# Kernel optimization log

Measured on AMD Instinct MI355X. Metric: run time of the kernel, lower is better.

Reference implementation:

```python
import jax, jax.numpy as jnp
import numpy as np

D_MODEL = 2048
NUM_HEADS = 16
D_Q = 1536
D_KV = 512
BS, SL = 2, 2048


def _lin(x, w, b):
    # torch nn.Linear: y = x @ w.T + b, w: [out, in]
    return jnp.einsum('...i,oi->...o', x, w) + b


def _freqs(seq_len, dim, theta=10000.0):
    # Faithful to source incl. precedence quirk: tn = 1 / ((theta ** arange) / dim).
    # float32 overflow -> inf -> tn = 0 for large exponents (identity rotation).
    exps = jnp.arange(0, dim, 2, dtype=jnp.float32)
    tn = 1.0 / ((theta ** exps) / dim)
    m = jnp.arange(seq_len, dtype=jnp.float32)
    ang = jnp.outer(m, tn)  # [sl, dim/2]
    return jnp.cos(ang), jnp.sin(ang)


def _rope(x, cos, sin):
    # x: [bs, sl, dim]; complex pairs are (x[..., 2i], x[..., 2i+1])
    xe = x[..., 0::2]
    xo = x[..., 1::2]
    re = xe * cos - xo * sin
    im = xe * sin + xo * cos
    return jnp.stack([re, im], axis=-1).reshape(x.shape)


def _init_linear(key, out_f, in_f):
    k1, k2 = jax.random.split(key)
    bound = 1.0 / np.sqrt(in_f)
    w = jax.random.uniform(k1, (out_f, in_f), jnp.float32, -bound, bound)
    b = jax.random.uniform(k2, (out_f,), jnp.float32, -bound, bound)
    return w, b


def setup_inputs() -> dict:
    key = jax.random.key(0)
    ks = jax.random.split(key, 9)
    x = jax.random.normal(ks[0], (BS, SL, D_MODEL), jnp.float32)
    w_down_q, b_down_q = _init_linear(ks[1], D_Q, D_MODEL)
    w_up_q, b_up_q = _init_linear(ks[2], D_MODEL, D_Q)
    w_down_kv, b_down_kv = _init_linear(ks[3], D_KV, D_MODEL)
    w_up_k, b_up_k = _init_linear(ks[4], D_MODEL, D_KV)
    w_up_v, b_up_v = _init_linear(ks[5], D_MODEL, D_KV)
    wq_r, bq_r = _init_linear(ks[6], D_MODEL, D_Q)
    wk_r, bk_r = _init_linear(ks[7], D_MODEL, D_KV)
    wo, bo = _init_linear(ks[8], D_MODEL, D_MODEL)
    return dict(x=x,
                w_down_q=w_down_q, b_down_q=b_down_q,
                w_up_q=w_up_q, b_up_q=b_up_q,
                w_down_kv=w_down_kv, b_down_kv=b_down_kv,
                w_up_k=w_up_k, b_up_k=b_up_k,
                w_up_v=w_up_v, b_up_v=b_up_v,
                wq_r=wq_r, bq_r=bq_r,
                wk_r=wk_r, bk_r=bk_r,
                wo=wo, bo=bo)


def reference(x, w_down_q, b_down_q, w_up_q, b_up_q, w_down_kv, b_down_kv,
              w_up_k, b_up_k, w_up_v, b_up_v, wq_r, bq_r, wk_r, bk_r, wo, bo):
    bs, sl, dim = x.shape
    nh, hd = NUM_HEADS, dim // NUM_HEADS
    cos, sin = _freqs(sl, dim)

    # Query path: down-proj -> up-proj content + decoupled RoPE branch
    ct_q = _lin(x, w_down_q, b_down_q)                       # [bs, sl, d_q]
    q_ct = _lin(ct_q, w_up_q, b_up_q)                        # [bs, sl, d_model]
    rope_q = _rope(_lin(ct_q, wq_r, bq_r), cos, sin)         # [bs, sl, d_model]
    q = (q_ct + rope_q).reshape(bs, sl, nh, hd)

    # KV path: shared latent -> separate K/V up-proj + RoPE branch on K
    ct_kv = _lin(x, w_down_kv, b_down_kv)                    # [bs, sl, d_kv]
    k_ct = _lin(ct_kv, w_up_k, b_up_k)
    rope_k = _rope(_lin(ct_kv, wk_r, bk_r), cos, sin)
    k = (k_ct + rope_k).reshape(bs, sl, nh, hd)
    v = _lin(ct_kv, w_up_v, b_up_v).reshape(bs, sl, nh, hd)

    # Attention: explicit matmul + softmax + matmul (no causal mask in source)
    scores = jnp.einsum('bqhd,bkhd->bhqk', q, k) / np.sqrt(hd)
    probs = jax.nn.softmax(scores, axis=-1)
    a = jnp.einsum('bhqk,bkhd->bqhd', probs, v).reshape(bs, sl, nh * hd)
    return _lin(a, wo, bo)
```

## Files before the change

kernel.cpp:

```cpp
#include <hip/hip_runtime.h>

typedef float f32x4 __attribute__((ext_vector_type(4)));
typedef float f32x16 __attribute__((ext_vector_type(16)));
typedef unsigned short us8 __attribute__((ext_vector_type(8)));

#define DEVINL __device__ __forceinline__

DEVINL unsigned short f2bf(float f) {
  unsigned u = __builtin_bit_cast(unsigned, f);
  u += 0x7fffu + ((u >> 16) & 1u);
  return (unsigned short)(u >> 16);
}
DEVINL float bf2f(unsigned short b) { return __builtin_bit_cast(float, ((unsigned)b) << 16); }
DEVINL us8 ld8(const unsigned short* p) { return *reinterpret_cast<const us8*>(p); }
DEVINL void mfma16(f32x4& acc, us8 a, us8 b) {
  asm("v_mfma_f32_16x16x32_bf16 %0, %1, %2, %0" : "+v"(acc) : "v"(a), "v"(b));
}
DEVINL void mfma32(f32x16& acc, us8 a, us8 b) {
  asm("v_mfma_f32_32x32x16_bf16 %0, %1, %2, %0" : "+v"(acc) : "v"(a), "v"(b));
}
DEVINL unsigned cvtpk_bf16(float lo, float hi) {
  unsigned r;
  asm("v_cvt_pk_bf16_f32 %0, %1, %2" : "=v"(r) : "v"(lo), "v"(hi));
  return r;
}
DEVINL us8 us8_from4(unsigned a, unsigned b, unsigned c, unsigned d) {
  union { unsigned u[4]; us8 v; } x;
  x.u[0] = a; x.u[1] = b; x.u[2] = c; x.u[3] = d;
  return x.v;
}
DEVINL void gld16(const void* g, void* l) {
  __builtin_amdgcn_global_load_lds((const __attribute__((address_space(1))) void*)g,
                                   (__attribute__((address_space(3))) void*)l, 16, 0, 0);
}

DEVINL void cvt4(const float* __restrict__ s, unsigned short* __restrict__ d, long i) {
  float4 v = reinterpret_cast<const float4*>(s)[i];
  unsigned lo = (unsigned)f2bf(v.x) | ((unsigned)f2bf(v.y) << 16);
  unsigned hi = (unsigned)f2bf(v.z) | ((unsigned)f2bf(v.w) << 16);
  reinterpret_cast<uint2*>(d)[i] = make_uint2(lo, hi);
}

__global__ void k_prep(const float* __restrict__ x, const float* __restrict__ wdq,
                       const float* __restrict__ wdkv, const float* __restrict__ wuq,
                       const float* __restrict__ wqr, const float* __restrict__ wuk,
                       const float* __restrict__ wkr, const float* __restrict__ wuv,
                       const float* __restrict__ wo, const float* __restrict__ bdq,
                       const float* __restrict__ bdkv, const float* __restrict__ buq,
                       const float* __restrict__ bqr, const float* __restrict__ buk,
                       const float* __restrict__ bkr, const float* __restrict__ buv,
                       unsigned short* __restrict__ xb, unsigned short* __restrict__ wcd,
                       unsigned short* __restrict__ wcq, unsigned short* __restrict__ wck,
                       unsigned short* __restrict__ wob, float* __restrict__ cosT,
                       float* __restrict__ sinT, float* __restrict__ bcd,
                       float* __restrict__ bcq, float* __restrict__ bck) {
  constexpr long C0 = 2097152, C1 = C0 + 786432, C2 = C1 + 262144, C3 = C2 + 786432,
                 C4 = C3 + 786432, C5 = C4 + 262144, C6 = C5 + 262144, C7 = C6 + 262144,
                 C8 = C7 + 1048576, C9 = C8 + 2097152, C10 = C9 + 3072;
  long u = (long)blockIdx.x * 256 + threadIdx.x;
  if (u < C0) cvt4(x, xb, u);
  else if (u < C1) cvt4(wdq, wcd, u - C0);
  else if (u < C2) cvt4(wdkv, wcd + 1536L * 2048, u - C1);
  else if (u < C3) cvt4(wuq, wcq, u - C2);
  else if (u < C4) cvt4(wqr, wcq + 2048L * 1536, u - C3);
  else if (u < C5) cvt4(wuk, wck, u - C4);
  else if (u < C6) cvt4(wkr, wck + 2048L * 512, u - C5);
  else if (u < C7) cvt4(wuv, wck + 4096L * 512, u - C6);
  else if (u < C8) cvt4(wo, wob, u - C7);
  else if (u < C9) {
    long idx = u - C8;
    int s = (int)(idx >> 10), i = (int)(idx & 1023);
    float e = (float)(2 * i);
    float pw = powf(10000.0f, e);
    float tn = 1.0f / (pw / 2048.0f);
    float ang = (float)s * tn;
    cosT[idx] = cosf(ang);
    sinT[idx] = sinf(ang);
  } else if (u < C10) {
    long j4 = (u - C9) * 4;
#pragma unroll
    for (int k = 0; k < 4; ++k) {
      long j = j4 + k;
      if (j < 2048) {
        bcd[j] = j < 1536 ? bdq[j] : bdkv[j - 1536];
      } else if (j < 6144) {
        long jj = j - 2048;
        bcq[jj] = jj < 2048 ? buq[jj] : bqr[jj - 2048];
      } else {
        long jj = j - 6144;
        bck[jj] = jj < 2048 ? buk[jj] : (jj < 4096 ? bkr[jj - 2048] : buv[jj - 4096]);
      }
    }
  }
}

template <int BN, bool OUTF32>
__global__ __launch_bounds__(BN) void k_gemm256(const unsigned short* __restrict__ A,
                                                const unsigned short* __restrict__ B,
                                                const float* __restrict__ bias,
                                                void* __restrict__ Cout, int N, int K, int lda) {
  constexpr int THREADS = BN;
  constexpr int WN = BN / 128;
  constexpr int NA = 512 / THREADS;
  constexpr int NB = BN * 4 / THREADS;
  constexpr int SLOT = 128 * 32 + BN * 32;
  __shared__ unsigned short lds[3 * SLOT];
  const int nwg = gridDim.x;
  const int orig = blockIdx.x;
  const int wgid = (orig & 7) * (nwg >> 3) + (orig >> 3);
  const int nbn = N / BN;
  const int bn = wgid % nbn, bm = wgid / nbn;
  const int tid = threadIdx.x, lane = tid & 63, w = tid >> 6;
  const int g = lane >> 4, l16 = lane & 15;
  const int wm = w / WN, wn = w % WN;
  f32x4 acc[4][8] = {};
  const unsigned short* Abase = A + (size_t)bm * 128 * lda;
  const unsigned short* Bbase = B + (size_t)bn * BN * K;
  size_t aoff[NA], boff[NB];
#pragma unroll
  for (int j = 0; j < NA; ++j) {
    int c = j * THREADS + tid;
    int row = c >> 2, gc = (c & 3) ^ ((row >> 1) & 3);
    aoff[j] = (size_t)row * lda + gc * 8;
  }
#pragma unroll
  for (int j = 0; j < NB; ++j) {
    int cb = j * THREADS + tid;
    int row = cb >> 2, gc = (cb & 3) ^ ((row >> 1) & 3);
    boff[j] = (size_t)row * K + gc * 8;
  }
  auto STAGE = [&](int slot, int kt) {
    unsigned short* s = &lds[slot * SLOT];
#pragma unroll
    for (int j = 0; j < NA; ++j) gld16(Abase + aoff[j] + kt, s + (j * THREADS + tid) * 8);
#pragma unroll
    for (int j = 0; j < NB; ++j)
      gld16(Bbase + boff[j] + kt, s + 128 * 32 + (j * THREADS + tid) * 8);
  };
  const int nt = K >> 5;
  STAGE(0, 0);
  STAGE(1, 32);
  if (BN == 256) asm volatile("s_waitcnt vmcnt(6)" ::: "memory");
  else           asm volatile("s_waitcnt vmcnt(8)" ::: "memory");
  asm volatile("s_barrier" ::: "memory");
  for (int t = 0; t < nt; ++t) {
    const int slot = t % 3;
    if (t + 2 < nt) STAGE((t + 2) % 3, (t + 2) * 32);
    const unsigned short* sa = &lds[slot * SLOT];
    const unsigned short* sb = sa + 128 * 32;
    us8 af[4], bf[8];
#pragma unroll
    for (int m = 0; m < 4; ++m) {
      int row = wm * 64 + m * 16 + l16;
      af[m] = ld8(&sa[row * 32 + ((g ^ ((row >> 1) & 3)) * 8)]);
    }
#pragma unroll
    for (int n = 0; n < 8; ++n) {
      int row = wn * 128 + n * 16 + l16;
      bf[n] = ld8(&sb[row * 32 + ((g ^ ((row >> 1) & 3)) * 8)]);
    }
    __builtin_amdgcn_s_setprio(1);
#pragma unroll
    for (int m = 0; m < 4; ++m)
#pragma unroll
      for (int n = 0; n < 8; ++n) mfma16(acc[m][n], af[m], bf[n]);
    __builtin_amdgcn_s_setprio(0);
    if (t < nt - 2) {
      if (BN == 256) asm volatile("s_waitcnt vmcnt(6)" ::: "memory");
      else           asm volatile("s_waitcnt vmcnt(8)" ::: "memory");
    } else {
      asm volatile("s_waitcnt vmcnt(0)" ::: "memory");
    }
    asm volatile("s_barrier" ::: "memory");
  }
#pragma unroll
  for (int n = 0; n < 8; ++n) {
    int col = bn * BN + wn * 128 + n * 16 + l16;
    float bv = bias[col];
#pragma unroll
    for (int m = 0; m < 4; ++m) {
      int row0 = bm * 128 + wm * 64 + m * 16 + g * 4;
#pragma unroll
      for (int r = 0; r < 4; ++r) {
        float vv = acc[m][n][r] + bv;
        if (OUTF32)
          reinterpret_cast<float*>(Cout)[(size_t)(row0 + r) * N + col] = vv;
        else
          reinterpret_cast<unsigned short*>(Cout)[(size_t)(row0 + r) * N + col] = f2bf(vv);
      }
    }
  }
}

__global__ void k_rope_combine(const unsigned short* __restrict__ src, int ldin,
                               const float* __restrict__ cosT, const float* __restrict__ sinT,
                               unsigned short* __restrict__ outp) {
  int pidx = blockIdx.x * 256 + threadIdx.x;
  if (pidx >= 4096 * 1024) return;
  int row = pidx >> 10, i = pidx & 1023;
  int s = row & 2047;
  float c = cosT[s * 1024 + i], sn = sinT[s * 1024 + i];
  const unsigned short* rp = src + (size_t)row * ldin;
  float xe = bf2f(rp[2048 + 2 * i]), xo = bf2f(rp[2048 + 2 * i + 1]);
  float re = xe * c - xo * sn;
  float im = xe * sn + xo * c;
  float q0 = bf2f(rp[2 * i]) + re;
  float q1 = bf2f(rp[2 * i + 1]) + im;
  unsigned pack = (unsigned)f2bf(q0) | ((unsigned)f2bf(q1) << 16);
  *reinterpret_cast<unsigned*>(&outp[(size_t)row * 2048 + 2 * i]) = pack;
}

__global__ __launch_bounds__(256) void k_transpose_v(const unsigned short* __restrict__ v, int ld,
                                                     unsigned short* __restrict__ vt) {
  __shared__ unsigned short t[32][33];
  int tx = threadIdx.x & 31, ty = threadIdx.x >> 5;
  int r0 = blockIdx.y * 32, c0 = blockIdx.x * 32;
#pragma unroll
  for (int jj = 0; jj < 4; ++jj)
    t[ty * 4 + jj][tx] = v[(size_t)(r0 + ty * 4 + jj) * ld + c0 + tx];
  __syncthreads();
  int b = r0 >> 11;
#pragma unroll
  for (int jj = 0; jj < 4; ++jj) {
    int colc = c0 + ty * 4 + jj;
    size_t orow = (size_t)(b * 16 + (colc >> 7)) * 128 + (colc & 127);
    vt[orow * 2048 + (r0 & 2047) + tx] = t[tx][ty * 4 + jj];
  }
}

__global__ __launch_bounds__(256, 2) void k_attn(const unsigned short* __restrict__ Qsrc,
                                                 const unsigned short* __restrict__ Kg,
                                                 const unsigned short* __restrict__ VT,
                                                 const float* __restrict__ cosT,
                                                 const float* __restrict__ sinT,
                                                 unsigned short* __restrict__ Aout) {
  __shared__ unsigned short Ks[2][64 * 128];
  __shared__ unsigned short VTs[2][128 * 64];
  const int tid = threadIdx.x, lane = tid & 63, w = tid >> 6;
  const int hh = lane >> 5, q32 = lane & 31;
  const int orig = blockIdx.x;
  const int wgid = (orig & 7) * 64 + (orig >> 3);
  const int qt = wgid & 15;
  const int hb = wgid >> 4;
  const int h = hb & 15, b = hb >> 4;
  const float SC2 = 0.08838834764831845f * 1.4426950408889634f;
  const int srow = qt * 128 + w * 32 + q32;
  us8 qf[8];
  {
    const unsigned short* Qr = Qsrc + ((size_t)b * 2048 + srow) * 4096;
#pragma unroll
    for (int ds = 0; ds < 8; ++ds) {
      int dcol = h * 128 + ds * 16 + hh * 8;
      us8 c8 = ld8(&Qr[dcol]);
      us8 r8 = ld8(&Qr[2048 + dcol]);
      unsigned wv[4];
#pragma unroll
      for (int p2 = 0; p2 < 4; ++p2) {
        int i = (dcol >> 1) + p2;
        float cc = cosT[srow * 1024 + i], ss = sinT[srow * 1024 + i];
        float xe = bf2f(r8[2 * p2]), xo = bf2f(r8[2 * p2 + 1]);
        float o0 = (bf2f(c8[2 * p2]) + xe * cc - xo * ss) * SC2;
        float o1 = (bf2f(c8[2 * p2 + 1]) + xe * ss + xo * cc) * SC2;
        wv[p2] = cvtpk_bf16(o0, o1);
      }
      qf[ds] = us8_from4(wv[0], wv[1], wv[2], wv[3]);
    }
  }
  f32x16 O[4] = {};
  float mq = -1e30f, lq = 0.f;
  const unsigned short* Kbase = Kg + (size_t)b * 2048 * 2048 + h * 128;
  const unsigned short* VTb = VT + (size_t)(b * 16 + h) * 128 * 2048;
  auto STAGE = [&](int bufi, int ktrow) {
#pragma unroll
    for (int j = 0; j < 4; ++j) {
      int ch = (j * 4 + w) * 64 + lane;
      int key = ch >> 4, cp = ch & 15;
      gld16(&Kbase[(size_t)(ktrow + key) * 2048 + (size_t)((cp ^ (key & 15)) * 8)],
            &Ks[bufi][(j * 4 + w) * 512]);
      int d = ch >> 3, c2 = ch & 7;
      gld16(&VTb[(size_t)d * 2048 + ktrow + (size_t)((c2 ^ (d & 7)) * 8)],
            &VTs[bufi][(j * 4 + w) * 512]);
    }
  };
  STAGE(0, 0);
  for (int t = 0; t < 32; ++t) {
    const int cur = t & 1;
    __syncthreads();
    if (t < 31) STAGE(cur ^ 1, (t + 1) * 64);
    f32x16 S2[2] = {};
    __builtin_amdgcn_s_setprio(1);
#pragma unroll
    for (int kb = 0; kb < 2; ++kb) {
      const int key = kb * 32 + q32;
      const int swz = key & 15;
#pragma unroll
      for (int ds = 0; ds < 8; ++ds) {
        us8 kf = ld8(&Ks[cur][key * 128 + (((ds * 2 + hh) ^ swz) * 8)]);
        mfma32(S2[kb], kf, qf[ds]);
      }
    }
    __builtin_amdgcn_s_setprio(0);
    float mx[16];
#pragma unroll
    for (int r = 0; r < 16; ++r) mx[r] = fmaxf(S2[0][r], S2[1][r]);
#pragma unroll
    for (int st = 8; st > 0; st >>= 1)
#pragma unroll
      for (int r = 0; r < st; ++r) mx[r] = fmaxf(mx[r], mx[r + st]);
    float smax = fmaxf(mx[0], __shfl_xor(mx[0], 32));
    if (!__all(smax <= mq + 8.0f)) {
      float mn = fmaxf(mq, smax);
      float fac = exp2f(mq - mn);
      lq *= fac;
      mq = mn;
#pragma unroll
      for (int r = 0; r < 16; ++r) {
        int qr = (r & 3) + 8 * (r >> 2) + 4 * hh;
        float fr = __shfl(fac, qr);
#pragma unroll
        for (int db = 0; db < 4; ++db) O[db][r] *= fr;
      }
    }
    float ps = 0.f;
    unsigned pk[2][8];
#pragma unroll
    for (int kb = 0; kb < 2; ++kb) {
      float e[16];
#pragma unroll
      for (int r = 0; r < 16; ++r) {
        e[r] = exp2f(S2[kb][r] - mq);
        ps += e[r];
      }
#pragma unroll
      for (int pp = 0; pp < 8; ++pp) pk[kb][pp] = cvtpk_bf16(e[2 * pp], e[2 * pp + 1]);
    }
    ps += __shfl_xor(ps, 32);
    lq += ps;
    __builtin_amdgcn_s_setprio(1);
#pragma unroll
    for (int ks = 0; ks < 4; ++ks) {
      const int kb = ks >> 1, kk = ks & 1;
      unsigned u_own = hh ? pk[kb][4 * kk + 2] : pk[kb][4 * kk + 0];
      unsigned v_own = hh ? pk[kb][4 * kk + 3] : pk[kb][4 * kk + 1];
      unsigned u_snd = hh ? pk[kb][4 * kk + 0] : pk[kb][4 * kk + 2];
      unsigned v_snd = hh ? pk[kb][4 * kk + 1] : pk[kb][4 * kk + 3];
      unsigned uo = (unsigned)__shfl_xor((int)u_snd, 32);
      unsigned vo = (unsigned)__shfl_xor((int)v_snd, 32);
      us8 pa = us8_from4(hh ? uo : u_own, hh ? vo : v_own, hh ? u_own : uo, hh ? v_own : vo);
#pragma unroll
      for (int db = 0; db < 4; ++db) {
        int d = db * 32 + q32;
        us8 vf = ld8(&VTs[cur][d * 64 + (((ks * 2 + hh) ^ (d & 7)) * 8)]);
        mfma32(O[db], pa, vf);
      }
    }
    __builtin_amdgcn_s_setprio(0);
  }
  float inv = 1.0f / lq;
#pragma unroll
  for (int r = 0; r < 16; ++r) {
    int qr = (r & 3) + 8 * (r >> 2) + 4 * hh;
    float ir = __shfl(inv, qr);
    size_t row = (size_t)b * 2048 + qt * 128 + w * 32 + qr;
#pragma unroll
    for (int db = 0; db < 4; ++db)
      Aout[row * 2048 + h * 128 + db * 32 + q32] = f2bf(O[db][r] * ir);
  }
}

extern "C" void kernel_launch(void* const* d_in, const int* in_sizes, int n_in, void* d_out,
                              int out_size, void* d_ws, size_t ws_size, hipStream_t stream) {
  (void)in_sizes; (void)n_in; (void)out_size; (void)ws_size;
  constexpr int Mr = 4096;
  using US = unsigned short;
  const float* x        = (const float*)d_in[0];
  const float* w_down_q = (const float*)d_in[1];
  const float* b_down_q = (const float*)d_in[2];
  const float* w_up_q   = (const float*)d_in[3];
  const float* b_up_q   = (const float*)d_in[4];
  const float* w_down_kv= (const float*)d_in[5];
  const float* b_down_kv= (const float*)d_in[6];
  const float* w_up_k   = (const float*)d_in[7];
  const float* b_up_k   = (const float*)d_in[8];
  const float* w_up_v   = (const float*)d_in[9];
  const float* b_up_v   = (const float*)d_in[10];
  const float* wq_r     = (const float*)d_in[11];
  const float* bq_r     = (const float*)d_in[12];
  const float* wk_r     = (const float*)d_in[13];
  const float* bk_r     = (const float*)d_in[14];
  const float* wo       = (const float*)d_in[15];
  const float* bo       = (const float*)d_in[16];

  char* p = (char*)d_ws;
  auto alloc = [&](size_t bytes) { char* r = p; p += (bytes + 255) & ~(size_t)255; return r; };
  float* cosT      = (float*)alloc((size_t)2048 * 1024 * 4);
  float* sinT      = (float*)alloc((size_t)2048 * 1024 * 4);
  US* wcat_kvup    = (US*)alloc((size_t)6144 * 512 * 2);
  US* wob          = (US*)alloc((size_t)2048 * 2048 * 2);
  US* ct           = (US*)alloc((size_t)Mr * 2048 * 2);
  US* t12          = (US*)alloc((size_t)Mr * 4096 * 2);
  US* vtb          = (US*)alloc((size_t)Mr * 2048 * 2);
  US* kb           = (US*)alloc((size_t)Mr * 2048 * 2);
  float* bcat_down = (float*)alloc(2048 * 4);
  float* bcat_qup  = (float*)alloc(4096 * 4);
  float* bcat_kvup = (float*)alloc(6144 * 4);
  US* xb           = (US*)alloc((size_t)Mr * 2048 * 2);
  US* wcat_down    = (US*)alloc((size_t)2048 * 2048 * 2);
  US* wcat_qup     = (US*)alloc((size_t)4096 * 1536 * 2);
  alloc((size_t)12 * 1024 * 1024);
  US* kv3  = xb;
  US* aout = ct;

  k_prep<<<dim3(33804), dim3(256), 0, stream>>>(
      x, w_down_q, w_down_kv, w_up_q, wq_r, w_up_k, wk_r, w_up_v, wo, b_down_q, b_down_kv,
      b_up_q, bq_r, b_up_k, bk_r, b_up_v, xb, wcat_down, wcat_qup, wcat_kvup, wob, cosT, sinT,
      bcat_down, bcat_qup, bcat_kvup);

  k_gemm256<128, false><<<dim3((2048 / 128) * (Mr / 128)), dim3(128), 0, stream>>>(
      xb, wcat_down, bcat_down, (void*)ct, 2048, 2048, 2048);
  k_gemm256<256, false><<<dim3((4096 / 256) * (Mr / 128)), dim3(256), 0, stream>>>(
      ct, wcat_qup, bcat_qup, (void*)t12, 4096, 1536, 2048);
  k_gemm256<256, false><<<dim3((6144 / 256) * (Mr / 128)), dim3(256), 0, stream>>>(
      ct + 1536, wcat_kvup, bcat_kvup, (void*)kv3, 6144, 512, 2048);
  k_rope_combine<<<dim3((4096 * 1024 + 255) / 256), dim3(256), 0, stream>>>(kv3, 6144, cosT, sinT,
                                                                            kb);
  k_transpose_v<<<dim3(64, 128), dim3(256), 0, stream>>>(kv3 + 4096, 6144, vtb);
  k_attn<<<dim3(512), dim3(256), 0, stream>>>(t12, kb, vtb, cosT, sinT, aout);
  k_gemm256<128, true><<<dim3((2048 / 128) * (Mr / 128)), dim3(128), 0, stream>>>(
      aout, wob, bo, d_out, 2048, 2048, 2048);
}
```

Measured before the change: 359.1 us.

## Split attention KV range across two workgroups and merge partial softmax results

The attention kernel is split along the key dimension into two halves, doubling the grid to 1024 workgroups. Each half writes unnormalized fp32 partial outputs plus running max and sum, and a new merge kernel combines them into bf16. LDS double buffering is replaced with a single buffer and an extra barrier, allowing up to 4 workgroups per CU. This adds fp32 partial-output traffic (written into d_out and kv3 scratch) and an extra launch, and staging loads are no longer overlapped with compute.

```diff
diff --git a/kernel.cpp b/kernel.cpp
--- a/kernel.cpp
+++ b/kernel.cpp
@@ -228,20 +228,24 @@
   }
 }
 
-__global__ __launch_bounds__(256, 2) void k_attn(const unsigned short* __restrict__ Qsrc,
+__global__ __launch_bounds__(256, 4) void k_attn(const unsigned short* __restrict__ Qsrc,
                                                  const unsigned short* __restrict__ Kg,
                                                  const unsigned short* __restrict__ VT,
                                                  const float* __restrict__ cosT,
                                                  const float* __restrict__ sinT,
-                                                 unsigned short* __restrict__ Aout) {
-  __shared__ unsigned short Ks[2][64 * 128];
-  __shared__ unsigned short VTs[2][128 * 64];
+                                                 float* __restrict__ Op0,
+                                                 float* __restrict__ Op1,
+                                                 float2* __restrict__ ml0,
+                                                 float2* __restrict__ ml1) {
+  __shared__ unsigned short Ks[64 * 128];
+  __shared__ unsigned short VTs[128 * 64];
   const int tid = threadIdx.x, lane = tid & 63, w = tid >> 6;
   const int hh = lane >> 5, q32 = lane & 31;
   const int orig = blockIdx.x;
-  const int wgid = (orig & 7) * 64 + (orig >> 3);
-  const int qt = wgid & 15;
-  const int hb = wgid >> 4;
+  const int wgid = (orig & 7) * 128 + (orig >> 3);
+  const int half = wgid & 1;
+  const int qt = (wgid >> 1) & 15;
+  const int hb = wgid >> 5;
   const int h = hb & 15, b = hb >> 4;
   const float SC2 = 0.08838834764831845f * 1.4426950408889634f;
   const int srow = qt * 128 + w * 32 + q32;
@@ -270,23 +274,23 @@
   float mq = -1e30f, lq = 0.f;
   const unsigned short* Kbase = Kg + (size_t)b * 2048 * 2048 + h * 128;
   const unsigned short* VTb = VT + (size_t)(b * 16 + h) * 128 * 2048;
-  auto STAGE = [&](int bufi, int ktrow) {
+  auto STAGE = [&](int ktrow) {
 #pragma unroll
     for (int j = 0; j < 4; ++j) {
       int ch = (j * 4 + w) * 64 + lane;
       int key = ch >> 4, cp = ch & 15;
       gld16(&Kbase[(size_t)(ktrow + key) * 2048 + (size_t)((cp ^ (key & 15)) * 8)],
-            &Ks[bufi][(j * 4 + w) * 512]);
+            &Ks[(j * 4 + w) * 512]);
       int d = ch >> 3, c2 = ch & 7;
       gld16(&VTb[(size_t)d * 2048 + ktrow + (size_t)((c2 ^ (d & 7)) * 8)],
-            &VTs[bufi][(j * 4 + w) * 512]);
+            &VTs[(j * 4 + w) * 512]);
     }
   };
-  STAGE(0, 0);
-  for (int t = 0; t < 32; ++t) {
-    const int cur = t & 1;
+  const int t0 = half * 16;
+  for (int tt = 0; tt < 16; ++tt) {
     __syncthreads();
-    if (t < 31) STAGE(cur ^ 1, (t + 1) * 64);
+    STAGE((t0 + tt) * 64);
+    __syncthreads();
     f32x16 S2[2] = {};
     __builtin_amdgcn_s_setprio(1);
 #pragma unroll
@@ -295,7 +299,7 @@
       const int swz = key & 15;
 #pragma unroll
       for (int ds = 0; ds < 8; ++ds) {
-        us8 kf = ld8(&Ks[cur][key * 128 + (((ds * 2 + hh) ^ swz) * 8)]);
+        us8 kf = ld8(&Ks[key * 128 + (((ds * 2 + hh) ^ swz) * 8)]);
         mfma32(S2[kb], kf, qf[ds]);
       }
     }
@@ -350,22 +354,46 @@
 #pragma unroll
       for (int db = 0; db < 4; ++db) {
         int d = db * 32 + q32;
-        us8 vf = ld8(&VTs[cur][d * 64 + (((ks * 2 + hh) ^ (d & 7)) * 8)]);
+        us8 vf = ld8(&VTs[d * 64 + (((ks * 2 + hh) ^ (d & 7)) * 8)]);
         mfma32(O[db], pa, vf);
       }
     }
     __builtin_amdgcn_s_setprio(0);
   }
-  float inv = 1.0f / lq;
+  float* Op = half ? Op1 : Op0;
+  const size_t rbase = (size_t)b * 2048 + qt * 128 + w * 32;
 #pragma unroll
   for (int r = 0; r < 16; ++r) {
     int qr = (r & 3) + 8 * (r >> 2) + 4 * hh;
-    float ir = __shfl(inv, qr);
-    size_t row = (size_t)b * 2048 + qt * 128 + w * 32 + qr;
 #pragma unroll
     for (int db = 0; db < 4; ++db)
-      Aout[row * 2048 + h * 128 + db * 32 + q32] = f2bf(O[db][r] * ir);
-  }
+      Op[(rbase + qr) * 2048 + h * 128 + db * 32 + q32] = O[db][r];
+  }
+  if (hh == 0) {
+    float2* ml = half ? ml1 : ml0;
+    ml[(rbase + q32) * 16 + h] = make_float2(mq, lq);
+  }
+}
+
+__global__ void k_merge(const float* __restrict__ Op0, const float* __restrict__ Op1,
+                        const float2* __restrict__ ml0, const float2* __restrict__ ml1,
+                        unsigned short* __restrict__ aout) {
+  int u = blockIdx.x * 256 + threadIdx.x;
+  int d4 = u & 31, h = (u >> 5) & 15;
+  long rg = u >> 9;
+  float2 a = ml0[rg * 16 + h], c = ml1[rg * 16 + h];
+  float m = fmaxf(a.x, c.x);
+  float w0 = exp2f(a.x - m), w1 = exp2f(c.x - m);
+  float inv = 1.0f / (a.y * w0 + c.y * w1);
+  long base = rg * 2048 + h * 128 + d4 * 4;
+  float4 o0 = *reinterpret_cast<const float4*>(&Op0[base]);
+  float4 o1 = *reinterpret_cast<const float4*>(&Op1[base]);
+  ushort4 r;
+  r.x = f2bf((o0.x * w0 + o1.x * w1) * inv);
+  r.y = f2bf((o0.y * w0 + o1.y * w1) * inv);
+  r.z = f2bf((o0.z * w0 + o1.z * w1) * inv);
+  r.w = f2bf((o0.w * w0 + o1.w * w1) * inv);
+  *reinterpret_cast<ushort4*>(&aout[base]) = r;
 }
 
 extern "C" void kernel_launch(void* const* d_in, const int* in_sizes, int n_in, void* d_out,
@@ -410,6 +438,10 @@
   alloc((size_t)12 * 1024 * 1024);
   US* kv3  = xb;
   US* aout = ct;
+  float*  Op0 = (float*)d_out;
+  float*  Op1 = (float*)kv3;
+  float2* ml0 = (float2*)((char*)kv3 + 33554432);
+  float2* ml1 = (float2*)((char*)kv3 + 33554432 + 524288);
 
   k_prep<<<dim3(33804), dim3(256), 0, stream>>>(
       x, w_down_q, w_down_kv, w_up_q, wq_r, w_up_k, wk_r, w_up_v, wo, b_down_q, b_down_kv,
@@ -425,7 +457,8 @@
   k_rope_combine<<<dim3((4096 * 1024 + 255) / 256), dim3(256), 0, stream>>>(kv3, 6144, cosT, sinT,
                                                                             kb);
   k_transpose_v<<<dim3(64, 128), dim3(256), 0, stream>>>(kv3 + 4096, 6144, vtb);
-  k_attn<<<dim3(512), dim3(256), 0, stream>>>(t12, kb, vtb, cosT, sinT, aout);
+  k_attn<<<dim3(1024), dim3(256), 0, stream>>>(t12, kb, vtb, cosT, sinT, Op0, Op1, ml0, ml1);
+  k_merge<<<dim3(8192), dim3(256), 0, stream>>>(Op0, Op1, ml0, ml1, aout);
   k_gemm256<128, true><<<dim3((2048 / 128) * (Mr / 128)), dim3(128), 0, stream>>>(
       aout, wob, bo, d_out, 2048, 2048, 2048);
 }
```

New measurement: 544.8 us. 51.7% more time.
